# Kernel optimization log

Measured on AMD Instinct MI355X. Metric: run time of the kernel, lower is better.

Reference implementation:

```python
import jax, jax.numpy as jnp
import numpy as np

D_MODEL = 1024
N_HEADS = 16
D_HEAD = D_MODEL // N_HEADS


def setup_inputs() -> dict:
    key = jax.random.key(0)
    k_x, k_qkv, k_out = jax.random.split(key, 3)
    x = jax.random.normal(k_x, (2, 2048, D_MODEL), dtype=jnp.float32)
    # nn.Linear weights: out = x @ W.T ; store as [out_features, in_features]
    s = 1.0 / np.sqrt(D_MODEL)
    w_qkv = jax.random.uniform(k_qkv, (3 * D_MODEL, D_MODEL), jnp.float32, -s, s)
    w_out = jax.random.uniform(k_out, (D_MODEL, D_MODEL), jnp.float32, -s, s)
    return {"x": x, "w_qkv": w_qkv, "w_out": w_out}


def reference(x, w_qkv, w_out):
    B, T, D = x.shape
    qkv = jnp.einsum("btd,ed->bte", x, w_qkv)  # [B,T,3D]
    q, k, v = jnp.split(qkv, 3, axis=-1)

    def heads(t):  # [B,T,D] -> [B,H,T,d]
        return t.reshape(B, T, N_HEADS, D_HEAD).transpose(0, 2, 1, 3)

    q, k, v = heads(q), heads(k), heads(v)
    scale = jnp.float32(np.sqrt(D_HEAD))
    scores = jnp.einsum("bhqd,bhkd->bhqk", q, k) / scale  # [B,H,T,T]
    causal = jnp.tril(jnp.ones((T, T), dtype=bool))  # True = keep
    scores = jnp.where(causal, scores, -jnp.inf)
    attn = jax.nn.softmax(scores, axis=-1)
    out = jnp.einsum("bhqk,bhkd->bhqd", attn, v)
    out = out.transpose(0, 2, 1, 3).reshape(B, T, D)
    return jnp.einsum("btd,ed->bte", out, w_out)
```

## Files before the change

kernel.cpp:

```cpp
#include <hip/hip_runtime.h>
#include <hip/hip_bf16.h>

typedef __attribute__((ext_vector_type(8))) short bf16x8;
typedef __attribute__((ext_vector_type(8))) unsigned short ushort8;
typedef __attribute__((ext_vector_type(4))) float f32x4;
typedef __attribute__((ext_vector_type(16))) float f32x16;

typedef const __attribute__((address_space(1))) void gvoid;
typedef __attribute__((address_space(3))) void svoid;

__device__ __forceinline__ unsigned short f2bf(float f) {
  union { float f; unsigned int u; } v; v.f = f;
  unsigned int u = v.u;
  unsigned int r = (u + 0x7fffu + ((u >> 16) & 1u)) >> 16;
  return (unsigned short)r;
}

__global__ void cast_kernel(const float* __restrict__ in, unsigned short* __restrict__ out, int n4) {
  int i = blockIdx.x * 256 + threadIdx.x;
  if (i < n4) {
    const float4 v = reinterpret_cast<const float4*>(in)[i];
    ushort4 o;
    o.x = f2bf(v.x); o.y = f2bf(v.y); o.z = f2bf(v.z); o.w = f2bf(v.w);
    reinterpret_cast<ushort4*>(out)[i] = o;
  }
}

template<bool OUT_BF16>
__global__ __launch_bounds__(256) void gemm_bt(const unsigned short* __restrict__ A,
                                               const unsigned short* __restrict__ B,
                                               void* __restrict__ Cv,
                                               int M, int N, int K,
                                               float qscale, int qcols) {
  constexpr int BM = 128, BK = 32;
  __shared__ alignas(16) unsigned short As[BM * BK];
  __shared__ alignas(16) unsigned short Bs[BM * BK];
  const int tid = threadIdx.x;
  const int l  = tid & 63;
  const int w  = tid >> 6;
  const int wr = w >> 1, wc = w & 1;
  const int lr = l & 15, lg = l >> 4;
  const long tile_m = (long)blockIdx.x * BM;
  const long tile_n = (long)blockIdx.y * BM;

  const int c0 = tid, c1 = tid + 256;
  const unsigned short* pa0 = A + (tile_m + (c0 >> 2)) * (long)K + (c0 & 3) * 8;
  const unsigned short* pa1 = A + (tile_m + (c1 >> 2)) * (long)K + (c1 & 3) * 8;
  const unsigned short* pb0 = B + (tile_n + (c0 >> 2)) * (long)K + (c0 & 3) * 8;
  const unsigned short* pb1 = B + (tile_n + (c1 >> 2)) * (long)K + (c1 & 3) * 8;
  unsigned short* lA0 = As + (w * 64) * 8;
  unsigned short* lA1 = As + (256 + w * 64) * 8;
  unsigned short* lB0 = Bs + (w * 64) * 8;
  unsigned short* lB1 = Bs + (256 + w * 64) * 8;

  f32x4 acc[4][4] = {};

  for (int k0 = 0; k0 < K; k0 += BK) {
    __syncthreads();
    __builtin_amdgcn_global_load_lds((gvoid*)(pa0 + k0), (svoid*)lA0, 16, 0, 0);
    __builtin_amdgcn_global_load_lds((gvoid*)(pa1 + k0), (svoid*)lA1, 16, 0, 0);
    __builtin_amdgcn_global_load_lds((gvoid*)(pb0 + k0), (svoid*)lB0, 16, 0, 0);
    __builtin_amdgcn_global_load_lds((gvoid*)(pb1 + k0), (svoid*)lB1, 16, 0, 0);
    __syncthreads();
    bf16x8 af[4], bfr[4];
#pragma unroll
    for (int m = 0; m < 4; ++m)
      af[m] = *reinterpret_cast<const bf16x8*>(As + (wr * 64 + m * 16 + lr) * BK + lg * 8);
#pragma unroll
    for (int n = 0; n < 4; ++n)
      bfr[n] = *reinterpret_cast<const bf16x8*>(Bs + (wc * 64 + n * 16 + lr) * BK + lg * 8);
#pragma unroll
    for (int m = 0; m < 4; ++m)
#pragma unroll
      for (int n = 0; n < 4; ++n)
        acc[m][n] = __builtin_amdgcn_mfma_f32_16x16x32_bf16(af[m], bfr[n], acc[m][n], 0, 0, 0);
  }

#pragma unroll
  for (int m = 0; m < 4; ++m)
#pragma unroll
    for (int n = 0; n < 4; ++n)
#pragma unroll
      for (int r = 0; r < 4; ++r) {
        long row = tile_m + wr * 64 + m * 16 + lg * 4 + r;
        long col = tile_n + wc * 64 + n * 16 + lr;
        float sc = (col < qcols) ? qscale : 1.0f;
        if (OUT_BF16)
          reinterpret_cast<unsigned short*>(Cv)[row * N + col] = f2bf(acc[m][n][r] * sc);
        else
          reinterpret_cast<float*>(Cv)[row * N + col] = acc[m][n][r] * sc;
      }
}

__global__ __launch_bounds__(256, 2) void attn_kernel(const unsigned short* __restrict__ qkv,
                                                      unsigned short* __restrict__ o) {
  constexpr int E = 3072, T = 2048;
  __shared__ alignas(16) unsigned short Ks[64 * 64];
  __shared__ alignas(16) unsigned short Vt[64 * 64];
  __shared__ float alBuf[4][32];
  const int tid = threadIdx.x;
  const int l = tid & 63, w = tid >> 6;
  const int hh = l >> 5;
  const int lc = l & 31;
  const int id = blockIdx.x;
  const int half = id >> 8, rr2 = id & 255;
  const int bx = rr2 & 15;
  const int bh = (rr2 >> 4) | (half << 4);
  const int qtb = half ? (15 - bx) : bx;
  const int b = bh >> 4, hd = bh & 15;
  const unsigned short* Qb = qkv + (size_t)b * T * E + hd * 64;
  const unsigned short* Kb = Qb + 1024;
  const unsigned short* Vb = Qb + 2048;

  const int qrow0 = qtb * 128 + w * 32;
  const int qg = qrow0 + lc;
  const int nt = 2 * qtb + 2;

  const int kr0 = tid >> 3, js0 = tid & 7;
  const int kr1 = kr0 + 32;
  const unsigned short* sK = Kb + (size_t)kr0 * E + js0 * 8;
  const unsigned short* sV = Vb + (size_t)kr0 * E + js0 * 8;
  const size_t tileStep = (size_t)64 * E;

  bf16x8 aq[4];
#pragma unroll
  for (int c = 0; c < 4; ++c)
    aq[c] = *reinterpret_cast<const bf16x8*>(Qb + (size_t)qg * E + c * 16 + hh * 8);

  f32x16 accO0 = {}, accO1 = {};
  float mL = -1e30f, ls = 0.f;

  ushort8 k0 = *reinterpret_cast<const ushort8*>(sK);
  ushort8 k1 = *reinterpret_cast<const ushort8*>(sK + 32 * E);
  ushort8 v0 = *reinterpret_cast<const ushort8*>(sV);
  ushort8 v1 = *reinterpret_cast<const ushort8*>(sV + 32 * E);

  for (int t = 0; t < nt; ++t) {
    __syncthreads();
    *reinterpret_cast<ushort8*>(Ks + kr0 * 64 + ((js0 ^ (kr0 & 7)) << 3)) = k0;
    *reinterpret_cast<ushort8*>(Ks + kr1 * 64 + ((js0 ^ (kr1 & 7)) << 3)) = k1;
#pragma unroll
    for (int e = 0; e < 8; ++e) {
      int d = js0 * 8 + e;
      int swz = (d ^ (d >> 3)) & 7;
      Vt[d * 64 + ((((kr0 >> 3) ^ swz) << 3) | (kr0 & 7))] = (unsigned short)v0[e];
      Vt[d * 64 + ((((kr1 >> 3) ^ swz) << 3) | (kr1 & 7))] = (unsigned short)v1[e];
    }
    __syncthreads();
    if (t + 1 < nt) {
      const unsigned short* nK = sK + (size_t)(t + 1) * tileStep;
      const unsigned short* nV = sV + (size_t)(t + 1) * tileStep;
      k0 = *reinterpret_cast<const ushort8*>(nK);
      k1 = *reinterpret_cast<const ushort8*>(nK + 32 * E);
      v0 = *reinterpret_cast<const ushort8*>(nV);
      v1 = *reinterpret_cast<const ushort8*>(nV + 32 * E);
    }

    if (t * 64 > qrow0 + 31) continue;

    f32x16 sT0 = {}, sT1 = {};
#pragma unroll
    for (int c = 0; c < 4; ++c) {
      int sl = ((2 * c + hh) ^ (lc & 7)) << 3;
      bf16x8 ak0 = *reinterpret_cast<const bf16x8*>(Ks + lc * 64 + sl);
      bf16x8 ak1 = *reinterpret_cast<const bf16x8*>(Ks + (32 + lc) * 64 + sl);
      sT0 = __builtin_amdgcn_mfma_f32_32x32x16_bf16(ak0, aq[c], sT0, 0, 0, 0);
      sT1 = __builtin_amdgcn_mfma_f32_32x32x16_bf16(ak1, aq[c], sT1, 0, 0, 0);
    }

    const bool needMask = (t * 64 + 63) > qrow0;
    float pm = -1e30f;
#pragma unroll
    for (int r = 0; r < 16; ++r) {
      int kb = t * 64 + (r & 3) + 8 * (r >> 2) + 4 * hh;
      float a0 = sT0[r], a1 = sT1[r];
      if (needMask) {
        if (kb > qg) a0 = -1e30f;
        if (kb + 32 > qg) a1 = -1e30f;
      }
      sT0[r] = a0; sT1[r] = a1;
      pm = fmaxf(pm, fmaxf(a0, a1));
    }
    pm = fmaxf(pm, __shfl_xor(pm, 32));

    if (__any(pm > mL + 8.f)) {
      float mn = fmaxf(mL, pm);
      float al = __expf(mL - mn);
      mL = mn;
      ls *= al;
      alBuf[w][lc] = al;
      asm volatile("s_waitcnt lgkmcnt(0)" ::: "memory");
      __builtin_amdgcn_sched_barrier(0);
#pragma unroll
      for (int r = 0; r < 16; ++r) {
        float alr = alBuf[w][(r & 3) + 8 * (r >> 2) + 4 * hh];
        accO0[r] *= alr;
        accO1[r] *= alr;
      }
    }

    bf16x8 pa[4];
    union U4 { unsigned int u[4]; bf16x8 v; };
#pragma unroll
    for (int n = 0; n < 2; ++n) {
      float p[16];
#pragma unroll
      for (int r = 0; r < 16; ++r) {
        float pv = __expf((n ? sT1[r] : sT0[r]) - mL);
        p[r] = pv;
        ls += pv;
      }
#pragma unroll
      for (int g = 0; g < 2; ++g) {
        unsigned int x0, x1, y0, y1;
        asm("v_cvt_pk_bf16_f32 %0, %1, %2" : "=v"(x0) : "v"(p[8 * g + 0]), "v"(p[8 * g + 1]));
        asm("v_cvt_pk_bf16_f32 %0, %1, %2" : "=v"(x1) : "v"(p[8 * g + 2]), "v"(p[8 * g + 3]));
        asm("v_cvt_pk_bf16_f32 %0, %1, %2" : "=v"(y0) : "v"(p[8 * g + 4]), "v"(p[8 * g + 5]));
        asm("v_cvt_pk_bf16_f32 %0, %1, %2" : "=v"(y1) : "v"(p[8 * g + 6]), "v"(p[8 * g + 7]));
        asm("v_permlane32_swap_b32 %0, %1" : "+v"(x0), "+v"(y0));
        asm("v_permlane32_swap_b32 %0, %1" : "+v"(x1), "+v"(y1));
        U4 fu;
        fu.u[0] = x0; fu.u[1] = x1; fu.u[2] = y0; fu.u[3] = y1;
        pa[2 * n + g] = fu.v;
      }
    }

#pragma unroll
    for (int cp = 0; cp < 4; ++cp) {
      int d0 = lc, d1 = 32 + lc;
      int sl0 = ((2 * cp + hh) ^ ((d0 ^ (d0 >> 3)) & 7)) << 3;
      int sl1 = ((2 * cp + hh) ^ ((d1 ^ (d1 >> 3)) & 7)) << 3;
      bf16x8 bv0 = *reinterpret_cast<const bf16x8*>(Vt + d0 * 64 + sl0);
      bf16x8 bv1 = *reinterpret_cast<const bf16x8*>(Vt + d1 * 64 + sl1);
      accO0 = __builtin_amdgcn_mfma_f32_32x32x16_bf16(pa[cp], bv0, accO0, 0, 0, 0);
      accO1 = __builtin_amdgcn_mfma_f32_32x32x16_bf16(pa[cp], bv1, accO1, 0, 0, 0);
    }
  }

  float inv = 1.f / (ls + __shfl_xor(ls, 32));
  alBuf[w][lc] = inv;
  asm volatile("s_waitcnt lgkmcnt(0)" ::: "memory");
  __builtin_amdgcn_sched_barrier(0);
#pragma unroll
  for (int r = 0; r < 16; ++r) {
    int q = (r & 3) + 8 * (r >> 2) + 4 * hh;
    float iv = alBuf[w][q];
    size_t row = (size_t)(b * T + qrow0 + q) * 1024 + hd * 64;
    o[row + lc]      = f2bf(accO0[r] * iv);
    o[row + 32 + lc] = f2bf(accO1[r] * iv);
  }
}

extern "C" void kernel_launch(void* const* d_in, const int* in_sizes, int n_in,
                              void* d_out, int out_size, void* d_ws, size_t ws_size,
                              hipStream_t stream) {
  const float* x     = (const float*)d_in[0];
  const float* w_qkv = (const float*)d_in[1];
  const float* w_out = (const float*)d_in[2];
  float* out = (float*)d_out;

  unsigned short* xb    = (unsigned short*)d_ws;
  unsigned short* wqkvb = xb    + (size_t)4096 * 1024;
  unsigned short* woutb = wqkvb + (size_t)3072 * 1024;
  unsigned short* qkv   = woutb + (size_t)1024 * 1024;
  unsigned short* attn  = qkv   + (size_t)4096 * 3072;

  cast_kernel<<<dim3(4096), 256, 0, stream>>>(x,     xb,    4096 * 1024 / 4);
  cast_kernel<<<dim3(3072), 256, 0, stream>>>(w_qkv, wqkvb, 3072 * 1024 / 4);
  cast_kernel<<<dim3(1024), 256, 0, stream>>>(w_out, woutb, 1024 * 1024 / 4);

  gemm_bt<true ><<<dim3(32, 24), 256, 0, stream>>>(xb,   wqkvb, (void*)qkv,  4096, 3072, 1024,
                                                   0.125f, 1024);
  attn_kernel  <<<dim3(512), 256, 0, stream>>>(qkv, attn);
  gemm_bt<false><<<dim3(32,  8), 256, 0, stream>>>(attn, woutb, (void*)out, 4096, 1024, 1024,
                                                   1.0f, 0);
}
```

Baseline: 127.3 us.

## Shrink attention blocks to 64 query rows with 2 waves, doubling grid

```diff
diff --git a/kernel.cpp b/kernel.cpp
--- a/kernel.cpp
+++ b/kernel.cpp
@@ -92,34 +92,34 @@
       }
 }
 
-__global__ __launch_bounds__(256, 2) void attn_kernel(const unsigned short* __restrict__ qkv,
+__global__ __launch_bounds__(128, 2) void attn_kernel(const unsigned short* __restrict__ qkv,
                                                       unsigned short* __restrict__ o) {
   constexpr int E = 3072, T = 2048;
   __shared__ alignas(16) unsigned short Ks[64 * 64];
   __shared__ alignas(16) unsigned short Vt[64 * 64];
-  __shared__ float alBuf[4][32];
+  __shared__ float alBuf[2][32];
   const int tid = threadIdx.x;
   const int l = tid & 63, w = tid >> 6;
   const int hh = l >> 5;
   const int lc = l & 31;
   const int id = blockIdx.x;
-  const int half = id >> 8, rr2 = id & 255;
-  const int bx = rr2 & 15;
-  const int bh = (rr2 >> 4) | (half << 4);
-  const int qtb = half ? (15 - bx) : bx;
+  const int g = id >> 8, j = id & 255;
+  const int bh = j & 31;
+  const int qp = j >> 5;
+  const int s = (g == 0) ? qp : (g == 1) ? (15 - qp) : (g == 2) ? (16 + qp) : (31 - qp);
   const int b = bh >> 4, hd = bh & 15;
   const unsigned short* Qb = qkv + (size_t)b * T * E + hd * 64;
   const unsigned short* Kb = Qb + 1024;
   const unsigned short* Vb = Qb + 2048;
 
-  const int qrow0 = qtb * 128 + w * 32;
+  const int qrow0 = s * 64 + w * 32;
   const int qg = qrow0 + lc;
-  const int nt = 2 * qtb + 2;
-
-  const int kr0 = tid >> 3, js0 = tid & 7;
-  const int kr1 = kr0 + 32;
-  const unsigned short* sK = Kb + (size_t)kr0 * E + js0 * 8;
-  const unsigned short* sV = Vb + (size_t)kr0 * E + js0 * 8;
+  const int nt = s + 1;
+
+  const int r0 = tid >> 3, js = tid & 7;
+  const unsigned short* sK = Kb + (size_t)r0 * E + js * 8;
+  const unsigned short* sV = Vb + (size_t)r0 * E + js * 8;
+  const size_t rowStep = (size_t)16 * E;
   const size_t tileStep = (size_t)64 * E;
 
   bf16x8 aq[4];
@@ -131,32 +131,47 @@
   float mL = -1e30f, ls = 0.f;
 
   ushort8 k0 = *reinterpret_cast<const ushort8*>(sK);
-  ushort8 k1 = *reinterpret_cast<const ushort8*>(sK + 32 * E);
+  ushort8 k1 = *reinterpret_cast<const ushort8*>(sK + rowStep);
+  ushort8 k2 = *reinterpret_cast<const ushort8*>(sK + 2 * rowStep);
+  ushort8 k3 = *reinterpret_cast<const ushort8*>(sK + 3 * rowStep);
   ushort8 v0 = *reinterpret_cast<const ushort8*>(sV);
-  ushort8 v1 = *reinterpret_cast<const ushort8*>(sV + 32 * E);
+  ushort8 v1 = *reinterpret_cast<const ushort8*>(sV + rowStep);
+  ushort8 v2 = *reinterpret_cast<const ushort8*>(sV + 2 * rowStep);
+  ushort8 v3 = *reinterpret_cast<const ushort8*>(sV + 3 * rowStep);
+
+  const int ksl = (js ^ (r0 & 7)) << 3;
+  const int krl = r0 & 7;
+  const int krh = r0 >> 3;
 
   for (int t = 0; t < nt; ++t) {
     __syncthreads();
-    *reinterpret_cast<ushort8*>(Ks + kr0 * 64 + ((js0 ^ (kr0 & 7)) << 3)) = k0;
-    *reinterpret_cast<ushort8*>(Ks + kr1 * 64 + ((js0 ^ (kr1 & 7)) << 3)) = k1;
+    *reinterpret_cast<ushort8*>(Ks + (r0     ) * 64 + ksl) = k0;
+    *reinterpret_cast<ushort8*>(Ks + (r0 + 16) * 64 + ksl) = k1;
+    *reinterpret_cast<ushort8*>(Ks + (r0 + 32) * 64 + ksl) = k2;
+    *reinterpret_cast<ushort8*>(Ks + (r0 + 48) * 64 + ksl) = k3;
 #pragma unroll
     for (int e = 0; e < 8; ++e) {
-      int d = js0 * 8 + e;
+      int d = js * 8 + e;
       int swz = (d ^ (d >> 3)) & 7;
-      Vt[d * 64 + ((((kr0 >> 3) ^ swz) << 3) | (kr0 & 7))] = (unsigned short)v0[e];
-      Vt[d * 64 + ((((kr1 >> 3) ^ swz) << 3) | (kr1 & 7))] = (unsigned short)v1[e];
+      unsigned short* vd = Vt + d * 64 + krl;
+      vd[(((krh    ) ^ swz) << 3)] = (unsigned short)v0[e];
+      vd[(((krh + 2) ^ swz) << 3)] = (unsigned short)v1[e];
+      vd[(((krh + 4) ^ swz) << 3)] = (unsigned short)v2[e];
+      vd[(((krh + 6) ^ swz) << 3)] = (unsigned short)v3[e];
     }
     __syncthreads();
     if (t + 1 < nt) {
       const unsigned short* nK = sK + (size_t)(t + 1) * tileStep;
       const unsigned short* nV = sV + (size_t)(t + 1) * tileStep;
       k0 = *reinterpret_cast<const ushort8*>(nK);
-      k1 = *reinterpret_cast<const ushort8*>(nK + 32 * E);
+      k1 = *reinterpret_cast<const ushort8*>(nK + rowStep);
+      k2 = *reinterpret_cast<const ushort8*>(nK + 2 * rowStep);
+      k3 = *reinterpret_cast<const ushort8*>(nK + 3 * rowStep);
       v0 = *reinterpret_cast<const ushort8*>(nV);
-      v1 = *reinterpret_cast<const ushort8*>(nV + 32 * E);
-    }
-
-    if (t * 64 > qrow0 + 31) continue;
+      v1 = *reinterpret_cast<const ushort8*>(nV + rowStep);
+      v2 = *reinterpret_cast<const ushort8*>(nV + 2 * rowStep);
+      v3 = *reinterpret_cast<const ushort8*>(nV + 3 * rowStep);
+    }
 
     f32x16 sT0 = {}, sT1 = {};
 #pragma unroll
@@ -211,17 +226,17 @@
         ls += pv;
       }
 #pragma unroll
-      for (int g = 0; g < 2; ++g) {
+      for (int gg = 0; gg < 2; ++gg) {
         unsigned int x0, x1, y0, y1;
-        asm("v_cvt_pk_bf16_f32 %0, %1, %2" : "=v"(x0) : "v"(p[8 * g + 0]), "v"(p[8 * g + 1]));
-        asm("v_cvt_pk_bf16_f32 %0, %1, %2" : "=v"(x1) : "v"(p[8 * g + 2]), "v"(p[8 * g + 3]));
-        asm("v_cvt_pk_bf16_f32 %0, %1, %2" : "=v"(y0) : "v"(p[8 * g + 4]), "v"(p[8 * g + 5]));
-        asm("v_cvt_pk_bf16_f32 %0, %1, %2" : "=v"(y1) : "v"(p[8 * g + 6]), "v"(p[8 * g + 7]));
+        asm("v_cvt_pk_bf16_f32 %0, %1, %2" : "=v"(x0) : "v"(p[8 * gg + 0]), "v"(p[8 * gg + 1]));
+        asm("v_cvt_pk_bf16_f32 %0, %1, %2" : "=v"(x1) : "v"(p[8 * gg + 2]), "v"(p[8 * gg + 3]));
+        asm("v_cvt_pk_bf16_f32 %0, %1, %2" : "=v"(y0) : "v"(p[8 * gg + 4]), "v"(p[8 * gg + 5]));
+        asm("v_cvt_pk_bf16_f32 %0, %1, %2" : "=v"(y1) : "v"(p[8 * gg + 6]), "v"(p[8 * gg + 7]));
         asm("v_permlane32_swap_b32 %0, %1" : "+v"(x0), "+v"(y0));
         asm("v_permlane32_swap_b32 %0, %1" : "+v"(x1), "+v"(y1));
         U4 fu;
         fu.u[0] = x0; fu.u[1] = x1; fu.u[2] = y0; fu.u[3] = y1;
-        pa[2 * n + g] = fu.v;
+        pa[2 * n + gg] = fu.v;
       }
     }
 
@@ -271,7 +286,7 @@
 
   gemm_bt<true ><<<dim3(32, 24), 256, 0, stream>>>(xb,   wqkvb, (void*)qkv,  4096, 3072, 1024,
                                                    0.125f, 1024);
-  attn_kernel  <<<dim3(512), 256, 0, stream>>>(qkv, attn);
+  attn_kernel  <<<dim3(1024), 128, 0, stream>>>(qkv, attn);
   gemm_bt<false><<<dim3(32,  8), 256, 0, stream>>>(attn, woutb, (void*)out, 4096, 1024, 1024,
                                                    1.0f, 0);
 }
```

After: 135.4 us. +6.4%, slower.

## Split attention KV tiles across two wave groups with in-block softmax merge

Applied to the files above, without the earlier changes.

```diff
diff --git a/kernel.cpp b/kernel.cpp
--- a/kernel.cpp
+++ b/kernel.cpp
@@ -92,16 +92,18 @@
       }
 }
 
-__global__ __launch_bounds__(256, 2) void attn_kernel(const unsigned short* __restrict__ qkv,
+__global__ __launch_bounds__(512, 4) void attn_kernel(const unsigned short* __restrict__ qkv,
                                                       unsigned short* __restrict__ o) {
   constexpr int E = 3072, T = 2048;
-  __shared__ alignas(16) unsigned short Ks[64 * 64];
-  __shared__ alignas(16) unsigned short Vt[64 * 64];
-  __shared__ float alBuf[4][32];
+  __shared__ alignas(16) unsigned short KVbuf[4][64 * 64];
+  __shared__ float alBuf[8][32];
+  __shared__ float mBufA[128], lBufA[128], mBufB[128], lBufB[128];
   const int tid = threadIdx.x;
   const int l = tid & 63, w = tid >> 6;
   const int hh = l >> 5;
   const int lc = l & 31;
+  const int wq = w & 3;
+  const int h2 = w >> 2;
   const int id = blockIdx.x;
   const int half = id >> 8, rr2 = id & 255;
   const int bx = rr2 & 15;
@@ -112,15 +114,20 @@
   const unsigned short* Kb = Qb + 1024;
   const unsigned short* Vb = Qb + 2048;
 
-  const int qrow0 = qtb * 128 + w * 32;
+  const int qrow0 = qtb * 128 + wq * 32;
   const int qg = qrow0 + lc;
   const int nt = 2 * qtb + 2;
-
-  const int kr0 = tid >> 3, js0 = tid & 7;
+  const int J = nt >> 1;
+
+  unsigned short* Ks = KVbuf[h2];
+  unsigned short* Vt = KVbuf[2 + h2];
+
+  const int st = tid & 255;
+  const int kr0 = st >> 3, js0 = st & 7;
   const int kr1 = kr0 + 32;
-  const unsigned short* sK = Kb + (size_t)kr0 * E + js0 * 8;
-  const unsigned short* sV = Vb + (size_t)kr0 * E + js0 * 8;
-  const size_t tileStep = (size_t)64 * E;
+  const unsigned short* sK = Kb + (size_t)(h2 * 64 + kr0) * E + js0 * 8;
+  const unsigned short* sV = Vb + (size_t)(h2 * 64 + kr0) * E + js0 * 8;
+  const size_t roundStep = (size_t)128 * E;
 
   bf16x8 aq[4];
 #pragma unroll
@@ -135,10 +142,13 @@
   ushort8 v0 = *reinterpret_cast<const ushort8*>(sV);
   ushort8 v1 = *reinterpret_cast<const ushort8*>(sV + 32 * E);
 
-  for (int t = 0; t < nt; ++t) {
+  const int ksl0 = (js0 ^ (kr0 & 7)) << 3;
+  const int ksl1 = (js0 ^ (kr1 & 7)) << 3;
+
+  for (int j = 0; j < J; ++j) {
     __syncthreads();
-    *reinterpret_cast<ushort8*>(Ks + kr0 * 64 + ((js0 ^ (kr0 & 7)) << 3)) = k0;
-    *reinterpret_cast<ushort8*>(Ks + kr1 * 64 + ((js0 ^ (kr1 & 7)) << 3)) = k1;
+    *reinterpret_cast<ushort8*>(Ks + kr0 * 64 + ksl0) = k0;
+    *reinterpret_cast<ushort8*>(Ks + kr1 * 64 + ksl1) = k1;
 #pragma unroll
     for (int e = 0; e < 8; ++e) {
       int d = js0 * 8 + e;
@@ -147,15 +157,16 @@
       Vt[d * 64 + ((((kr1 >> 3) ^ swz) << 3) | (kr1 & 7))] = (unsigned short)v1[e];
     }
     __syncthreads();
-    if (t + 1 < nt) {
-      const unsigned short* nK = sK + (size_t)(t + 1) * tileStep;
-      const unsigned short* nV = sV + (size_t)(t + 1) * tileStep;
+    if (2 * j + 2 + h2 < nt) {
+      const unsigned short* nK = sK + (size_t)(j + 1) * roundStep;
+      const unsigned short* nV = sV + (size_t)(j + 1) * roundStep;
       k0 = *reinterpret_cast<const ushort8*>(nK);
       k1 = *reinterpret_cast<const ushort8*>(nK + 32 * E);
       v0 = *reinterpret_cast<const ushort8*>(nV);
       v1 = *reinterpret_cast<const ushort8*>(nV + 32 * E);
     }
 
+    const int t = 2 * j + h2;
     if (t * 64 > qrow0 + 31) continue;
 
     f32x16 sT0 = {}, sT1 = {};
@@ -211,17 +222,17 @@
         ls += pv;
       }
 #pragma unroll
-      for (int g = 0; g < 2; ++g) {
+      for (int gg = 0; gg < 2; ++gg) {
         unsigned int x0, x1, y0, y1;
-        asm("v_cvt_pk_bf16_f32 %0, %1, %2" : "=v"(x0) : "v"(p[8 * g + 0]), "v"(p[8 * g + 1]));
-        asm("v_cvt_pk_bf16_f32 %0, %1, %2" : "=v"(x1) : "v"(p[8 * g + 2]), "v"(p[8 * g + 3]));
-        asm("v_cvt_pk_bf16_f32 %0, %1, %2" : "=v"(y0) : "v"(p[8 * g + 4]), "v"(p[8 * g + 5]));
-        asm("v_cvt_pk_bf16_f32 %0, %1, %2" : "=v"(y1) : "v"(p[8 * g + 6]), "v"(p[8 * g + 7]));
+        asm("v_cvt_pk_bf16_f32 %0, %1, %2" : "=v"(x0) : "v"(p[8 * gg + 0]), "v"(p[8 * gg + 1]));
+        asm("v_cvt_pk_bf16_f32 %0, %1, %2" : "=v"(x1) : "v"(p[8 * gg + 2]), "v"(p[8 * gg + 3]));
+        asm("v_cvt_pk_bf16_f32 %0, %1, %2" : "=v"(y0) : "v"(p[8 * gg + 4]), "v"(p[8 * gg + 5]));
+        asm("v_cvt_pk_bf16_f32 %0, %1, %2" : "=v"(y1) : "v"(p[8 * gg + 6]), "v"(p[8 * gg + 7]));
         asm("v_permlane32_swap_b32 %0, %1" : "+v"(x0), "+v"(y0));
         asm("v_permlane32_swap_b32 %0, %1" : "+v"(x1), "+v"(y1));
         U4 fu;
         fu.u[0] = x0; fu.u[1] = x1; fu.u[2] = y0; fu.u[3] = y1;
-        pa[2 * n + g] = fu.v;
+        pa[2 * n + gg] = fu.v;
       }
     }
 
@@ -237,17 +248,38 @@
     }
   }
 
-  float inv = 1.f / (ls + __shfl_xor(ls, 32));
-  alBuf[w][lc] = inv;
-  asm volatile("s_waitcnt lgkmcnt(0)" ::: "memory");
-  __builtin_amdgcn_sched_barrier(0);
-#pragma unroll
-  for (int r = 0; r < 16; ++r) {
-    int q = (r & 3) + 8 * (r >> 2) + 4 * hh;
-    float iv = alBuf[w][q];
-    size_t row = (size_t)(b * T + qrow0 + q) * 1024 + hd * 64;
-    o[row + lc]      = f2bf(accO0[r] * iv);
-    o[row + 32 + lc] = f2bf(accO1[r] * iv);
+  __syncthreads();
+  float lsTot = ls + __shfl_xor(ls, 32);
+  float* cb = (float*)KVbuf;
+  if (h2 == 1) {
+    if (hh == 0) { mBufB[wq * 32 + lc] = mL; lBufB[wq * 32 + lc] = lsTot; }
+#pragma unroll
+    for (int r = 0; r < 16; ++r) {
+      int q = (r & 3) + 8 * (r >> 2) + 4 * hh;
+      int row = wq * 32 + q;
+      cb[row * 64 + lc]      = accO0[r];
+      cb[row * 64 + 32 + lc] = accO1[r];
+    }
+  } else {
+    if (hh == 0) { mBufA[wq * 32 + lc] = mL; lBufA[wq * 32 + lc] = lsTot; }
+  }
+  __syncthreads();
+  if (h2 == 0) {
+#pragma unroll
+    for (int r = 0; r < 16; ++r) {
+      int q = (r & 3) + 8 * (r >> 2) + 4 * hh;
+      int row = wq * 32 + q;
+      float mA = mBufA[row], lA = lBufA[row];
+      float mB = mBufB[row], lB = lBufB[row];
+      float mS = fmaxf(mA, mB);
+      float eA = __expf(mA - mS), eB = __expf(mB - mS);
+      float inv = 1.f / (lA * eA + lB * eB);
+      float o0 = (accO0[r] * eA + cb[row * 64 + lc] * eB) * inv;
+      float o1 = (accO1[r] * eA + cb[row * 64 + 32 + lc] * eB) * inv;
+      size_t orow = (size_t)(b * T + qtb * 128 + row) * 1024 + hd * 64;
+      o[orow + lc]      = f2bf(o0);
+      o[orow + 32 + lc] = f2bf(o1);
+    }
   }
 }
 
@@ -271,7 +303,7 @@
 
   gemm_bt<true ><<<dim3(32, 24), 256, 0, stream>>>(xb,   wqkvb, (void*)qkv,  4096, 3072, 1024,
                                                    0.125f, 1024);
-  attn_kernel  <<<dim3(512), 256, 0, stream>>>(qkv, attn);
+  attn_kernel  <<<dim3(512), 512, 0, stream>>>(qkv, attn);
   gemm_bt<false><<<dim3(32,  8), 256, 0, stream>>>(attn, woutb, (void*)out, 4096, 1024, 1024,
                                                    1.0f, 0);
 }
```

Measured after the change: 161.6 us. 26.9% more time.

## Double-buffer GEMM LDS tiles and merge three cast kernels into one

Applied to the files above, without the earlier changes.

```diff
diff --git a/kernel.cpp b/kernel.cpp
--- a/kernel.cpp
+++ b/kernel.cpp
@@ -16,13 +16,22 @@
   return (unsigned short)r;
 }
 
-__global__ void cast_kernel(const float* __restrict__ in, unsigned short* __restrict__ out, int n4) {
-  int i = blockIdx.x * 256 + threadIdx.x;
-  if (i < n4) {
-    const float4 v = reinterpret_cast<const float4*>(in)[i];
-    ushort4 o;
-    o.x = f2bf(v.x); o.y = f2bf(v.y); o.z = f2bf(v.z); o.w = f2bf(v.w);
-    reinterpret_cast<ushort4*>(out)[i] = o;
+__global__ void cast3_kernel(const float* __restrict__ a, int na4,
+                             const float* __restrict__ b, int nb4,
+                             const float* __restrict__ c, int nc4,
+                             unsigned short* __restrict__ oa,
+                             unsigned short* __restrict__ ob,
+                             unsigned short* __restrict__ oc) {
+  const int total = na4 + nb4 + nc4;
+  for (int i = blockIdx.x * 256 + threadIdx.x; i < total; i += gridDim.x * 256) {
+    const float* src; unsigned short* dst; int j = i;
+    if (j < na4) { src = a; dst = oa; }
+    else if (j < na4 + nb4) { j -= na4; src = b; dst = ob; }
+    else { j -= na4 + nb4; src = c; dst = oc; }
+    const float4 v = reinterpret_cast<const float4*>(src)[j];
+    ushort4 o4;
+    o4.x = f2bf(v.x); o4.y = f2bf(v.y); o4.z = f2bf(v.z); o4.w = f2bf(v.w);
+    reinterpret_cast<ushort4*>(dst)[j] = o4;
   }
 }
 
@@ -32,9 +41,9 @@
                                                void* __restrict__ Cv,
                                                int M, int N, int K,
                                                float qscale, int qcols) {
-  constexpr int BM = 128, BK = 32;
-  __shared__ alignas(16) unsigned short As[BM * BK];
-  __shared__ alignas(16) unsigned short Bs[BM * BK];
+  constexpr int BM = 128, BK = 32, TILE = BM * BK;
+  __shared__ alignas(16) unsigned short As[2 * TILE];
+  __shared__ alignas(16) unsigned short Bs[2 * TILE];
   const int tid = threadIdx.x;
   const int l  = tid & 63;
   const int w  = tid >> 6;
@@ -48,32 +57,42 @@
   const unsigned short* pa1 = A + (tile_m + (c1 >> 2)) * (long)K + (c1 & 3) * 8;
   const unsigned short* pb0 = B + (tile_n + (c0 >> 2)) * (long)K + (c0 & 3) * 8;
   const unsigned short* pb1 = B + (tile_n + (c1 >> 2)) * (long)K + (c1 & 3) * 8;
-  unsigned short* lA0 = As + (w * 64) * 8;
-  unsigned short* lA1 = As + (256 + w * 64) * 8;
-  unsigned short* lB0 = Bs + (w * 64) * 8;
-  unsigned short* lB1 = Bs + (256 + w * 64) * 8;
+  const int woff = w * 512;
 
   f32x4 acc[4][4] = {};
 
+  __builtin_amdgcn_global_load_lds((gvoid*)pa0, (svoid*)(As + woff), 16, 0, 0);
+  __builtin_amdgcn_global_load_lds((gvoid*)pa1, (svoid*)(As + 2048 + woff), 16, 0, 0);
+  __builtin_amdgcn_global_load_lds((gvoid*)pb0, (svoid*)(Bs + woff), 16, 0, 0);
+  __builtin_amdgcn_global_load_lds((gvoid*)pb1, (svoid*)(Bs + 2048 + woff), 16, 0, 0);
+  __syncthreads();
+
+  int cur = 0;
   for (int k0 = 0; k0 < K; k0 += BK) {
-    __syncthreads();
-    __builtin_amdgcn_global_load_lds((gvoid*)(pa0 + k0), (svoid*)lA0, 16, 0, 0);
-    __builtin_amdgcn_global_load_lds((gvoid*)(pa1 + k0), (svoid*)lA1, 16, 0, 0);
-    __builtin_amdgcn_global_load_lds((gvoid*)(pb0 + k0), (svoid*)lB0, 16, 0, 0);
-    __builtin_amdgcn_global_load_lds((gvoid*)(pb1 + k0), (svoid*)lB1, 16, 0, 0);
-    __syncthreads();
+    if (k0 + BK < K) {
+      unsigned short* An = As + (cur ^ 1) * TILE;
+      unsigned short* Bn = Bs + (cur ^ 1) * TILE;
+      __builtin_amdgcn_global_load_lds((gvoid*)(pa0 + k0 + BK), (svoid*)(An + woff), 16, 0, 0);
+      __builtin_amdgcn_global_load_lds((gvoid*)(pa1 + k0 + BK), (svoid*)(An + 2048 + woff), 16, 0, 0);
+      __builtin_amdgcn_global_load_lds((gvoid*)(pb0 + k0 + BK), (svoid*)(Bn + woff), 16, 0, 0);
+      __builtin_amdgcn_global_load_lds((gvoid*)(pb1 + k0 + BK), (svoid*)(Bn + 2048 + woff), 16, 0, 0);
+    }
+    const unsigned short* AsC = As + cur * TILE;
+    const unsigned short* BsC = Bs + cur * TILE;
     bf16x8 af[4], bfr[4];
 #pragma unroll
     for (int m = 0; m < 4; ++m)
-      af[m] = *reinterpret_cast<const bf16x8*>(As + (wr * 64 + m * 16 + lr) * BK + lg * 8);
+      af[m] = *reinterpret_cast<const bf16x8*>(AsC + (wr * 64 + m * 16 + lr) * BK + lg * 8);
 #pragma unroll
     for (int n = 0; n < 4; ++n)
-      bfr[n] = *reinterpret_cast<const bf16x8*>(Bs + (wc * 64 + n * 16 + lr) * BK + lg * 8);
+      bfr[n] = *reinterpret_cast<const bf16x8*>(BsC + (wc * 64 + n * 16 + lr) * BK + lg * 8);
 #pragma unroll
     for (int m = 0; m < 4; ++m)
 #pragma unroll
       for (int n = 0; n < 4; ++n)
         acc[m][n] = __builtin_amdgcn_mfma_f32_16x16x32_bf16(af[m], bfr[n], acc[m][n], 0, 0, 0);
+    __syncthreads();
+    cur ^= 1;
   }
 
 #pragma unroll
@@ -211,17 +230,17 @@
         ls += pv;
       }
 #pragma unroll
-      for (int g = 0; g < 2; ++g) {
+      for (int gg = 0; gg < 2; ++gg) {
         unsigned int x0, x1, y0, y1;
-        asm("v_cvt_pk_bf16_f32 %0, %1, %2" : "=v"(x0) : "v"(p[8 * g + 0]), "v"(p[8 * g + 1]));
-        asm("v_cvt_pk_bf16_f32 %0, %1, %2" : "=v"(x1) : "v"(p[8 * g + 2]), "v"(p[8 * g + 3]));
-        asm("v_cvt_pk_bf16_f32 %0, %1, %2" : "=v"(y0) : "v"(p[8 * g + 4]), "v"(p[8 * g + 5]));
-        asm("v_cvt_pk_bf16_f32 %0, %1, %2" : "=v"(y1) : "v"(p[8 * g + 6]), "v"(p[8 * g + 7]));
+        asm("v_cvt_pk_bf16_f32 %0, %1, %2" : "=v"(x0) : "v"(p[8 * gg + 0]), "v"(p[8 * gg + 1]));
+        asm("v_cvt_pk_bf16_f32 %0, %1, %2" : "=v"(x1) : "v"(p[8 * gg + 2]), "v"(p[8 * gg + 3]));
+        asm("v_cvt_pk_bf16_f32 %0, %1, %2" : "=v"(y0) : "v"(p[8 * gg + 4]), "v"(p[8 * gg + 5]));
+        asm("v_cvt_pk_bf16_f32 %0, %1, %2" : "=v"(y1) : "v"(p[8 * gg + 6]), "v"(p[8 * gg + 7]));
         asm("v_permlane32_swap_b32 %0, %1" : "+v"(x0), "+v"(y0));
         asm("v_permlane32_swap_b32 %0, %1" : "+v"(x1), "+v"(y1));
         U4 fu;
         fu.u[0] = x0; fu.u[1] = x1; fu.u[2] = y0; fu.u[3] = y1;
-        pa[2 * n + g] = fu.v;
+        pa[2 * n + gg] = fu.v;
       }
     }
 
@@ -265,9 +284,10 @@
   unsigned short* qkv   = woutb + (size_t)1024 * 1024;
   unsigned short* attn  = qkv   + (size_t)4096 * 3072;
 
-  cast_kernel<<<dim3(4096), 256, 0, stream>>>(x,     xb,    4096 * 1024 / 4);
-  cast_kernel<<<dim3(3072), 256, 0, stream>>>(w_qkv, wqkvb, 3072 * 1024 / 4);
-  cast_kernel<<<dim3(1024), 256, 0, stream>>>(w_out, woutb, 1024 * 1024 / 4);
+  cast3_kernel<<<dim3(2048), 256, 0, stream>>>(x,     4096 * 1024 / 4,
+                                               w_qkv, 3072 * 1024 / 4,
+                                               w_out, 1024 * 1024 / 4,
+                                               xb, wqkvb, woutb);
 
   gemm_bt<true ><<<dim3(32, 24), 256, 0, stream>>>(xb,   wqkvb, (void*)qkv,  4096, 3072, 1024,
                                                    0.125f, 1024);
```

Result: faster. 116.8 us (-8.3%).
